# Kernel tuning notes

Measured on AMD Instinct MI355X. Metric: run time of the kernel, lower is better.

## Reference

```python
import jax, jax.numpy as jnp
import numpy as np

N_NODES = 100000
N_FEAT = 512
HIDDEN = 128
N_CLASS = 16
N_EDGES = 3200000
ALPHA = 0.25
N_ITERS = 2


def setup_inputs() -> dict:
    key = jax.random.key(0)
    k1, k2, k3, k4, k5 = jax.random.split(key, 5)
    x = jax.random.normal(k1, (N_NODES, N_FEAT), dtype=jnp.float32)
    W1 = jax.random.normal(k2, (N_FEAT, HIDDEN), dtype=jnp.float32) * 0.05
    W2 = jax.random.normal(k3, (HIDDEN, N_CLASS), dtype=jnp.float32) * 0.05
    edge_src = jax.random.randint(k4, (N_EDGES,), 0, N_NODES, dtype=jnp.int32)
    edge_dst = jax.random.randint(k5, (N_EDGES,), 0, N_NODES, dtype=jnp.int32)
    return {"x": x, "W1": W1, "W2": W2, "edge_src": edge_src, "edge_dst": edge_dst}


def reference(x, W1, W2, edge_src, edge_dst):
    # 2-layer GCN features
    hidden_1 = jax.nn.relu(x @ W1)                       # [N, H]
    local_logits = hidden_1 @ W2                         # [N, C]
    # degree of each row of adj (unit edge weights)
    deg = jax.ops.segment_sum(
        jnp.ones_like(edge_src, dtype=x.dtype), edge_src, num_segments=N_NODES
    )                                                    # [N]
    scale = (1.0 - ALPHA) / jnp.maximum(deg, 1e-12)      # [N]
    logits = local_logits
    for _ in range(N_ITERS):
        # SpMM: (adj @ logits)[i] = sum_{(i,j) in E} logits[j]
        agg = jax.ops.segment_sum(logits[edge_dst], edge_src, num_segments=N_NODES)
        logits = scale[:, None] * agg + ALPHA * local_logits
    return jax.nn.log_softmax(logits, axis=1)
```

## Files before the change

### kernel.cpp

```cpp
#include <hip/hip_runtime.h>
#include <math.h>

#define N_NODES 100000
#define N_FEAT  512
#define HIDDEN  128
#define N_CLASS 16
#define N_EDGES 3200000
#define ALPHA   0.25f

#define NB   782
#define CAP  5120
#define TILE 8192
#define NTB  391

typedef __attribute__((ext_vector_type(8))) short short8;
typedef __attribute__((ext_vector_type(4))) float float4v;

__device__ inline short f2b(float f) {
    union { float f; unsigned u; } c; c.f = f;
    unsigned r = c.u + 0x7FFF + ((c.u >> 16) & 1);
    return (short)(r >> 16);
}

__global__ void prep_kernel(const float* __restrict__ W1, const float* __restrict__ W2,
                            short* __restrict__ W1t, short* __restrict__ W2t,
                            int* __restrict__ cursor) {
    int t = blockIdx.x * 256 + threadIdx.x;
    if (t < N_FEAT * HIDDEN) {
        int k = t & 511, n = t >> 9;
        W1t[t] = f2b(W1[(size_t)k * HIDDEN + n]);
    }
    int t2 = t - N_FEAT * HIDDEN;
    if (t2 >= 0 && t2 < HIDDEN * N_CLASS) {
        int k = t2 & 127, n = t2 >> 7;
        W2t[t2] = f2b(W2[(size_t)k * N_CLASS + n]);
    }
    if (t < NB) cursor[t] = t * CAP;
}

__global__ __launch_bounds__(256) void mlp_mfma(const float* __restrict__ x,
                                                const short* __restrict__ W1t,
                                                const short* __restrict__ W2t,
                                                float* __restrict__ local_out,
                                                unsigned short* __restrict__ Lbf) {
    __shared__ __align__(16) short As[128 * 32];
    __shared__ __align__(16) short Bts[128 * 32];
    __shared__ __align__(16) short Hs[128 * 136];
    __shared__ __align__(16) short W2ts[16 * 136];

    const int tid  = threadIdx.x;
    const int wave = tid >> 6;
    const int wl   = tid & 63;
    const int lane15 = wl & 15;
    const int quad   = wl >> 4;
    const long block_row = (long)blockIdx.x * 128;

    {
        int n = tid >> 4, koff = (tid & 15) * 8;
        *(short8*)&W2ts[n * 136 + koff] = *(const short8*)&W2t[n * 128 + koff];
    }

    float4v acc[4][4];
#pragma unroll
    for (int i = 0; i < 4; ++i)
#pragma unroll
        for (int j = 0; j < 4; ++j) acc[i][j] = (float4v){0.f, 0.f, 0.f, 0.f};

    const int wr0 = (wave >> 1) * 64;
    const int wc0 = (wave & 1) * 64;

    for (int k0 = 0; k0 < N_FEAT; k0 += 32) {
#pragma unroll
        for (int l = 0; l < 2; ++l) {
            int c = tid + l * 256;
            int row = c >> 2, off = (c & 3) * 8;
            long grow = block_row + row;
            float4 v0 = make_float4(0.f, 0.f, 0.f, 0.f), v1 = v0;
            if (grow < N_NODES) {
                const float* p = x + grow * N_FEAT + k0 + off;
                v0 = *(const float4*)p;
                v1 = *(const float4*)(p + 4);
            }
            short8 h;
            h[0] = f2b(v0.x); h[1] = f2b(v0.y); h[2] = f2b(v0.z); h[3] = f2b(v0.w);
            h[4] = f2b(v1.x); h[5] = f2b(v1.y); h[6] = f2b(v1.z); h[7] = f2b(v1.w);
            *(short8*)&As[row * 32 + off] = h;
        }
#pragma unroll
        for (int l = 0; l < 2; ++l) {
            int c = tid + l * 256;
            int n = c >> 2, koff = (c & 3) * 8;
            *(short8*)&Bts[n * 32 + koff] = *(const short8*)&W1t[n * 512 + k0 + koff];
        }
        __syncthreads();

        short8 af[4], bfr[4];
#pragma unroll
        for (int i = 0; i < 4; ++i)
            af[i] = *(short8*)&As[(wr0 + i * 16 + lane15) * 32 + quad * 8];
#pragma unroll
        for (int j = 0; j < 4; ++j)
            bfr[j] = *(short8*)&Bts[(wc0 + j * 16 + lane15) * 32 + quad * 8];
#pragma unroll
        for (int i = 0; i < 4; ++i)
#pragma unroll
            for (int j = 0; j < 4; ++j)
                acc[i][j] = __builtin_amdgcn_mfma_f32_16x16x32_bf16(af[i], bfr[j], acc[i][j], 0, 0, 0);
        __syncthreads();
    }

#pragma unroll
    for (int i = 0; i < 4; ++i)
#pragma unroll
        for (int j = 0; j < 4; ++j)
#pragma unroll
            for (int r = 0; r < 4; ++r) {
                int row = wr0 + i * 16 + quad * 4 + r;
                int colh = wc0 + j * 16 + lane15;
                Hs[row * 136 + colh] = f2b(fmaxf(acc[i][j][r], 0.f));
            }
    __syncthreads();

    float4v acc2[2];
    acc2[0] = (float4v){0.f, 0.f, 0.f, 0.f};
    acc2[1] = acc2[0];
#pragma unroll
    for (int ks = 0; ks < 4; ++ks) {
        short8 a0 = *(short8*)&Hs[(wave * 32 + lane15) * 136 + ks * 32 + quad * 8];
        short8 a1 = *(short8*)&Hs[(wave * 32 + 16 + lane15) * 136 + ks * 32 + quad * 8];
        short8 b  = *(short8*)&W2ts[lane15 * 136 + ks * 32 + quad * 8];
        acc2[0] = __builtin_amdgcn_mfma_f32_16x16x32_bf16(a0, b, acc2[0], 0, 0, 0);
        acc2[1] = __builtin_amdgcn_mfma_f32_16x16x32_bf16(a1, b, acc2[1], 0, 0, 0);
    }
#pragma unroll
    for (int i2 = 0; i2 < 2; ++i2)
#pragma unroll
        for (int r = 0; r < 4; ++r) {
            long grow = block_row + wave * 32 + i2 * 16 + quad * 4 + r;
            if (grow < N_NODES) {
                float v = acc2[i2][r];
                local_out[grow * N_CLASS + lane15] = v;
                Lbf[grow * N_CLASS + lane15] = (unsigned short)f2b(v);
            }
        }
}

__global__ __launch_bounds__(256) void partition_kernel(const int* __restrict__ src,
                                                        const int* __restrict__ dst,
                                                        int* __restrict__ cursor,
                                                        unsigned* __restrict__ bbuf) {
    __shared__ unsigned sbuf[TILE];
    __shared__ unsigned short sbkt[TILE];
    __shared__ int cnt[1024];
    __shared__ int off[1024];
    __shared__ int gbase[NB];
    __shared__ int psum[256];

    const int tid = threadIdx.x;
    const int e0 = blockIdx.x * TILE;
    int n = N_EDGES - e0; if (n > TILE) n = TILE;

    for (int i = tid; i < 1024; i += 256) cnt[i] = 0;
    __syncthreads();

    unsigned pk[32]; int br[32];
#pragma unroll
    for (int k = 0; k < 32; ++k) {
        int i = tid + k * 256;
        br[k] = -1;
        if (i < n) {
            int s = src[e0 + i], d = dst[e0 + i];
            int b = s >> 7;
            int r = atomicAdd(&cnt[b], 1);
            pk[k] = ((unsigned)(s & 127) << 17) | (unsigned)d;
            br[k] = (b << 13) | r;
        }
    }
    __syncthreads();

    int b4 = tid * 4;
    int c0 = cnt[b4], c1 = cnt[b4 + 1], c2 = cnt[b4 + 2], c3 = cnt[b4 + 3];
    int tsum = c0 + c1 + c2 + c3;
    psum[tid] = tsum;
    __syncthreads();
    for (int o = 1; o < 256; o <<= 1) {
        int t = (tid >= o) ? psum[tid - o] : 0;
        __syncthreads();
        psum[tid] += t;
        __syncthreads();
    }
    int run = psum[tid] - tsum;
    off[b4] = run; off[b4 + 1] = run + c0;
    off[b4 + 2] = run + c0 + c1; off[b4 + 3] = run + c0 + c1 + c2;
    __syncthreads();

    for (int b = tid; b < NB; b += 256) {
        int c = cnt[b];
        if (c > 0) gbase[b] = atomicAdd(&cursor[b], c);
    }

#pragma unroll
    for (int k = 0; k < 32; ++k) {
        if (br[k] >= 0) {
            int b = br[k] >> 13, r = br[k] & 8191;
            int slot = off[b] + r;
            sbuf[slot] = pk[k];
            sbkt[slot] = (unsigned short)b;
        }
    }
    __syncthreads();

    for (int i = tid; i < n; i += 256) {
        int b = sbkt[i];
        bbuf[gbase[b] + (i - off[b])] = sbuf[i];
    }
}

__global__ __launch_bounds__(512) void bucket_sort(unsigned* __restrict__ bbuf,
                                                   const int* __restrict__ cursor,
                                                   int* __restrict__ row_start,
                                                   int* __restrict__ row_end,
                                                   float* __restrict__ scale) {
    __shared__ unsigned ein[CAP];
    __shared__ unsigned eout[CAP];
    __shared__ int cnt[128], ssc[128], cur[128];

    const int b = blockIdx.x;
    const int tid = threadIdx.x;
    const int base = b * CAP;
    int n = cursor[b] - base; if (n > CAP) n = CAP;

    for (int i = tid; i < n; i += 512) ein[i] = bbuf[base + i];
    if (tid < 128) cnt[tid] = 0;
    __syncthreads();

    for (int i = tid; i < n; i += 512) atomicAdd(&cnt[ein[i] >> 17], 1);
    __syncthreads();

    int v = (tid < 128) ? cnt[tid] : 0;
    if (tid < 128) ssc[tid] = v;
    __syncthreads();
    for (int o = 1; o < 128; o <<= 1) {
        int t = (tid >= o && tid < 128) ? ssc[tid - o] : 0;
        __syncthreads();
        if (tid < 128) ssc[tid] += t;
        __syncthreads();
    }
    if (tid < 128) cur[tid] = ssc[tid] - v;
    __syncthreads();

    for (int i = tid; i < n; i += 512) {
        unsigned u = ein[i];
        int r = atomicAdd(&cur[u >> 17], 1);
        eout[r] = u & 0x1FFFFu;
    }
    __syncthreads();

    for (int i = tid; i < n; i += 512) bbuf[base + i] = eout[i];

    if (tid < 128) {
        int node = (b << 7) + tid;
        if (node < N_NODES) {
            int st = base + ssc[tid] - v;
            row_start[node] = st;
            row_end[node]   = st + v;
            scale[node] = (1.0f - ALPHA) / fmaxf((float)v, 1e-12f);
        }
    }
}

template <int PASS>
__global__ __launch_bounds__(512) void spmm_csr(const unsigned* __restrict__ col,
                                                const int* __restrict__ row_start,
                                                const int* __restrict__ row_end,
                                                const float* __restrict__ scale,
                                                const unsigned short* __restrict__ Ltab,
                                                const float* __restrict__ local,
                                                unsigned short* __restrict__ out_bf,
                                                float* __restrict__ out_f32) {
    int t = blockIdx.x * 512 + threadIdx.x;
    int node = t >> 1;
    int half = t & 1;
    if (node >= N_NODES) return;
    const int rs = row_start[node], re = row_end[node];

    float acc[8];
#pragma unroll
    for (int k = 0; k < 8; ++k) acc[k] = 0.f;

    for (int base = rs; base < re; base += 16) {
        int cc[16];
#pragma unroll
        for (int j = 0; j < 16; ++j)
            cc[j] = (base + j < re) ? (int)col[base + j] : -1;
        uint4 g[16];
#pragma unroll
        for (int j = 0; j < 16; ++j) {
            int c = (cc[j] < 0) ? 0 : cc[j];
            g[j] = *(const uint4*)&Ltab[(size_t)c * N_CLASS + half * 8];
        }
#pragma unroll
        for (int j = 0; j < 16; ++j) {
            if (cc[j] >= 0) {
                union { unsigned u; float f; } w;
                w.u = g[j].x << 16;          acc[0] += w.f;
                w.u = g[j].x & 0xFFFF0000u;  acc[1] += w.f;
                w.u = g[j].y << 16;          acc[2] += w.f;
                w.u = g[j].y & 0xFFFF0000u;  acc[3] += w.f;
                w.u = g[j].z << 16;          acc[4] += w.f;
                w.u = g[j].z & 0xFFFF0000u;  acc[5] += w.f;
                w.u = g[j].w << 16;          acc[6] += w.f;
                w.u = g[j].w & 0xFFFF0000u;  acc[7] += w.f;
            }
        }
    }

    const float sc = scale[node];
    const float* lp = &local[(size_t)node * N_CLASS + half * 8];
    float4 l0 = *(const float4*)lp;
    float4 l1 = *(const float4*)(lp + 4);
    float r[8];
    r[0] = sc * acc[0] + ALPHA * l0.x; r[1] = sc * acc[1] + ALPHA * l0.y;
    r[2] = sc * acc[2] + ALPHA * l0.z; r[3] = sc * acc[3] + ALPHA * l0.w;
    r[4] = sc * acc[4] + ALPHA * l1.x; r[5] = sc * acc[5] + ALPHA * l1.y;
    r[6] = sc * acc[6] + ALPHA * l1.z; r[7] = sc * acc[7] + ALPHA * l1.w;

    if (PASS == 1) {
        uint4 o;
        o.x = ((unsigned)(unsigned short)f2b(r[1]) << 16) | (unsigned)(unsigned short)f2b(r[0]);
        o.y = ((unsigned)(unsigned short)f2b(r[3]) << 16) | (unsigned)(unsigned short)f2b(r[2]);
        o.z = ((unsigned)(unsigned short)f2b(r[5]) << 16) | (unsigned)(unsigned short)f2b(r[4]);
        o.w = ((unsigned)(unsigned short)f2b(r[7]) << 16) | (unsigned)(unsigned short)f2b(r[6]);
        *(uint4*)&out_bf[(size_t)node * N_CLASS + half * 8] = o;
    } else {
        float mx = r[0];
#pragma unroll
        for (int k = 1; k < 8; ++k) mx = fmaxf(mx, r[k]);
        mx = fmaxf(mx, __shfl_xor(mx, 1));
        float sm = 0.f;
#pragma unroll
        for (int k = 0; k < 8; ++k) sm += expf(r[k] - mx);
        sm += __shfl_xor(sm, 1);
        float ls = logf(sm) + mx;
        float4 o0 = make_float4(r[0] - ls, r[1] - ls, r[2] - ls, r[3] - ls);
        float4 o1 = make_float4(r[4] - ls, r[5] - ls, r[6] - ls, r[7] - ls);
        float* op = &out_f32[(size_t)node * N_CLASS + half * 8];
        *(float4*)op = o0;
        *(float4*)(op + 4) = o1;
    }
}

extern "C" void kernel_launch(void* const* d_in, const int* in_sizes, int n_in,
                              void* d_out, int out_size, void* d_ws, size_t ws_size,
                              hipStream_t stream) {
    const float* x    = (const float*)d_in[0];
    const float* W1   = (const float*)d_in[1];
    const float* W2   = (const float*)d_in[2];
    const int*   esrc = (const int*)d_in[3];
    const int*   edst = (const int*)d_in[4];
    float* out = (float*)d_out;
    char*  ws  = (char*)d_ws;

    float*          local   = (float*)         (ws + 0);
    unsigned short* Lbf     = (unsigned short*)(ws + 6400000);
    unsigned short* P1bf    = (unsigned short*)(ws + 9600000);
    float*          scale   = (float*)         (ws + 12800000);
    int*            rstart  = (int*)           (ws + 13200000);
    int*            rend    = (int*)           (ws + 13600000);
    short*          W1t     = (short*)         (ws + 14000000);
    short*          W2t     = (short*)         (ws + 14131072);
    int*            cursor  = (int*)           (ws + 14135168);
    unsigned*       bbuf    = (unsigned*)      (ws + 14138296);

    prep_kernel<<<(N_FEAT * HIDDEN + HIDDEN * N_CLASS + 255) / 256, 256, 0, stream>>>(W1, W2, W1t, W2t, cursor);
    mlp_mfma<<<(N_NODES + 127) / 128, 256, 0, stream>>>(x, W1t, W2t, local, Lbf);

    partition_kernel<<<NTB, 256, 0, stream>>>(esrc, edst, cursor, bbuf);
    bucket_sort<<<NB, 512, 0, stream>>>(bbuf, cursor, rstart, rend, scale);

    const int sgrid = (N_NODES * 2 + 511) / 512;
    spmm_csr<1><<<sgrid, 512, 0, stream>>>(bbuf, rstart, rend, scale, Lbf,  local, P1bf, nullptr);
    spmm_csr<2><<<sgrid, 512, 0, stream>>>(bbuf, rstart, rend, scale, P1bf, local, nullptr, out);
}
```

Before: 433.8 us.

## Load GEMM tiles via direct global-to-LDS async copies and vectorize CSR column loads

The MLP GEMM now stages fp32 x tiles and bf16 W1 tiles straight into LDS with global_load_lds 16-byte copies, using an XOR-swizzled layout. The fp32-to-bf16 conversion moves to the LDS-read side, and the H buffer is aliased onto the same shared memory. This is meant to cut register staging and VGPR pressure on the global-load path, at the price of twice the LDS footprint for A and conversion work repeated per wave. The SpMM column-index reads become aligned 16-byte vector loads with range masking, and bbuf is shifted to a 16-byte aligned offset so those loads are legal.

```diff
diff --git a/kernel.cpp b/kernel.cpp
--- a/kernel.cpp
+++ b/kernel.cpp
@@ -20,6 +20,12 @@
     union { float f; unsigned u; } c; c.f = f;
     unsigned r = c.u + 0x7FFF + ((c.u >> 16) & 1);
     return (short)(r >> 16);
+}
+
+__device__ __forceinline__ void async_copy16(void* l, const void* g) {
+    __builtin_amdgcn_global_load_lds(
+        (const __attribute__((address_space(1))) void*)g,
+        (__attribute__((address_space(3))) void*)l, 16, 0, 0);
 }
 
 __global__ void prep_kernel(const float* __restrict__ W1, const float* __restrict__ W2,
@@ -43,10 +49,12 @@
                                                 const short* __restrict__ W2t,
                                                 float* __restrict__ local_out,
                                                 unsigned short* __restrict__ Lbf) {
-    __shared__ __align__(16) short As[128 * 32];
-    __shared__ __align__(16) short Bts[128 * 32];
-    __shared__ __align__(16) short Hs[128 * 136];
+    __shared__ __align__(16) char uS[34816];
     __shared__ __align__(16) short W2ts[16 * 136];
+
+    float* const Asf = (float*)uS;
+    short* const Bt  = (short*)(uS + 16384);
+    short* const Hs  = (short*)uS;
 
     const int tid  = threadIdx.x;
     const int wave = tid >> 6;
@@ -69,38 +77,46 @@
     const int wr0 = (wave >> 1) * 64;
     const int wc0 = (wave & 1) * 64;
 
+    const int a_rsub = wl >> 3;
+    const int a_cch  = (wl & 7) ^ a_rsub;
+    const int b_rsub = wl >> 2;
+    const int b_cch  = (wl & 3) ^ ((wl >> 3) & 3);
+    char* const aBase = uS + wave * 4096;
+    char* const bBase = uS + 16384 + wave * 2048;
+
+    const int r7 = lane15 & 7;
+    const int rb = (lane15 >> 1) & 3;
+
     for (int k0 = 0; k0 < N_FEAT; k0 += 32) {
 #pragma unroll
-        for (int l = 0; l < 2; ++l) {
-            int c = tid + l * 256;
-            int row = c >> 2, off = (c & 3) * 8;
-            long grow = block_row + row;
-            float4 v0 = make_float4(0.f, 0.f, 0.f, 0.f), v1 = v0;
-            if (grow < N_NODES) {
-                const float* p = x + grow * N_FEAT + k0 + off;
-                v0 = *(const float4*)p;
-                v1 = *(const float4*)(p + 4);
-            }
+        for (int c = 0; c < 4; ++c) {
+            long gr = block_row + wave * 32 + c * 8 + a_rsub;
+            if (gr > N_NODES - 1) gr = N_NODES - 1;
+            async_copy16(aBase + c * 1024, x + gr * N_FEAT + k0 + a_cch * 4);
+        }
+#pragma unroll
+        for (int c = 0; c < 2; ++c) {
+            int rr = wave * 32 + c * 16 + b_rsub;
+            async_copy16(bBase + c * 1024, W1t + rr * 512 + k0 + b_cch * 8);
+        }
+        __syncthreads();
+
+        short8 af[4], bfr[4];
+#pragma unroll
+        for (int i = 0; i < 4; ++i) {
+            const float* pa = Asf + (wr0 + i * 16 + lane15) * 32;
+            float4 va = *(const float4*)(pa + (((2 * quad) ^ r7) << 2));
+            float4 vb = *(const float4*)(pa + (((2 * quad + 1) ^ r7) << 2));
             short8 h;
-            h[0] = f2b(v0.x); h[1] = f2b(v0.y); h[2] = f2b(v0.z); h[3] = f2b(v0.w);
-            h[4] = f2b(v1.x); h[5] = f2b(v1.y); h[6] = f2b(v1.z); h[7] = f2b(v1.w);
-            *(short8*)&As[row * 32 + off] = h;
-        }
-#pragma unroll
-        for (int l = 0; l < 2; ++l) {
-            int c = tid + l * 256;
-            int n = c >> 2, koff = (c & 3) * 8;
-            *(short8*)&Bts[n * 32 + koff] = *(const short8*)&W1t[n * 512 + k0 + koff];
-        }
-        __syncthreads();
-
-        short8 af[4], bfr[4];
-#pragma unroll
-        for (int i = 0; i < 4; ++i)
-            af[i] = *(short8*)&As[(wr0 + i * 16 + lane15) * 32 + quad * 8];
-#pragma unroll
-        for (int j = 0; j < 4; ++j)
-            bfr[j] = *(short8*)&Bts[(wc0 + j * 16 + lane15) * 32 + quad * 8];
+            h[0] = f2b(va.x); h[1] = f2b(va.y); h[2] = f2b(va.z); h[3] = f2b(va.w);
+            h[4] = f2b(vb.x); h[5] = f2b(vb.y); h[6] = f2b(vb.z); h[7] = f2b(vb.w);
+            af[i] = h;
+        }
+#pragma unroll
+        for (int j = 0; j < 4; ++j) {
+            const short* pb = Bt + (wc0 + j * 16 + lane15) * 32;
+            bfr[j] = *(const short8*)(pb + ((quad ^ rb) << 3));
+        }
 #pragma unroll
         for (int i = 0; i < 4; ++i)
 #pragma unroll
@@ -288,11 +304,21 @@
 #pragma unroll
     for (int k = 0; k < 8; ++k) acc[k] = 0.f;
 
-    for (int base = rs; base < re; base += 16) {
+    for (int base = rs & ~3; base < re; base += 16) {
+        const uint4 q0 = *(const uint4*)&col[base];
+        const uint4 q1 = *(const uint4*)&col[base + 4];
+        const uint4 q2 = *(const uint4*)&col[base + 8];
+        const uint4 q3 = *(const uint4*)&col[base + 12];
         int cc[16];
-#pragma unroll
-        for (int j = 0; j < 16; ++j)
-            cc[j] = (base + j < re) ? (int)col[base + j] : -1;
+        cc[0]  = (int)q0.x; cc[1]  = (int)q0.y; cc[2]  = (int)q0.z; cc[3]  = (int)q0.w;
+        cc[4]  = (int)q1.x; cc[5]  = (int)q1.y; cc[6]  = (int)q1.z; cc[7]  = (int)q1.w;
+        cc[8]  = (int)q2.x; cc[9]  = (int)q2.y; cc[10] = (int)q2.z; cc[11] = (int)q2.w;
+        cc[12] = (int)q3.x; cc[13] = (int)q3.y; cc[14] = (int)q3.z; cc[15] = (int)q3.w;
+#pragma unroll
+        for (int j = 0; j < 16; ++j) {
+            int idx = base + j;
+            if (idx < rs || idx >= re) cc[j] = -1;
+        }
         uint4 g[16];
 #pragma unroll
         for (int j = 0; j < 16; ++j) {
@@ -370,7 +396,7 @@
     short*          W1t     = (short*)         (ws + 14000000);
     short*          W2t     = (short*)         (ws + 14131072);
     int*            cursor  = (int*)           (ws + 14135168);
-    unsigned*       bbuf    = (unsigned*)      (ws + 14138296);
+    unsigned*       bbuf    = (unsigned*)      (ws + 14138368);
 
     prep_kernel<<<(N_FEAT * HIDDEN + HIDDEN * N_CLASS + 255) / 256, 256, 0, stream>>>(W1, W2, W1t, W2t, cursor);
     mlp_mfma<<<(N_NODES + 127) / 128, 256, 0, stream>>>(x, W1t, W2t, local, Lbf);
```

Measured after the change: 414.9 us. 4.4% less time.
